# Performance work log

Measured on AMD Instinct MI355X. Metric: run time of the kernel, lower is better.

The kernel has to match this reference:

```python
import jax, jax.numpy as jnp
import numpy as np

N_NODES = 50000


def _gcn_conv(x, W, b, src, dst, n):
    # PyG GCNConv: h = x @ W, symmetric-normalized aggregation, then + bias.
    h = x @ W  # [N, out]
    deg = jax.ops.segment_sum(jnp.ones_like(dst, dtype=h.dtype), dst, num_segments=n)
    dinv = jnp.where(deg > 0, jax.lax.rsqrt(jnp.maximum(deg, 1e-12)), 0.0)
    norm = dinv[src] * dinv[dst]  # [E]
    msg = h[src] * norm[:, None]  # gather + scale, [E, out]
    out = jax.ops.segment_sum(msg, dst, num_segments=n)
    return out + b


def setup_inputs() -> dict:
    key = jax.random.key(0)
    ks = jax.random.split(key, 8)
    d_in, d_h, d_out = 256, 256, 128
    E = 800000
    x = jax.random.normal(ks[0], (N_NODES, d_in), dtype=jnp.float32)
    edge_index = jax.random.randint(ks[1], (2, E), 0, N_NODES, dtype=jnp.int64)
    def glorot(k, shape):
        lim = np.sqrt(6.0 / (shape[0] + shape[1]))
        return jax.random.uniform(k, shape, jnp.float32, -lim, lim)
    return {
        "x": x,
        "edge_index": edge_index,
        "W1": glorot(ks[2], (d_in, d_h)), "b1": jnp.zeros((d_h,), jnp.float32),
        "W2": glorot(ks[3], (d_h, d_h)), "b2": jnp.zeros((d_h,), jnp.float32),
        "W3": glorot(ks[4], (d_h, d_out)), "b3": jnp.zeros((d_out,), jnp.float32),
    }


def reference(x, edge_index, W1, b1, W2, b2, W3, b3):
    n = x.shape[0]
    # add self-loops once (PyG GCNConv default add_self_loops=True)
    loop = jnp.arange(n, dtype=edge_index.dtype)
    src = jnp.concatenate([edge_index[0], loop])
    dst = jnp.concatenate([edge_index[1], loop])
    h = _gcn_conv(x, W1, b1, src, dst, n)
    h = jax.nn.relu(h)  # dropout is identity in eval mode
    h = _gcn_conv(h, W2, b2, src, dst, n)
    h = jax.nn.relu(h)
    h = _gcn_conv(h, W3, b3, src, dst, n)
    return h
```

## Files before the change

### kernel.cpp

```cpp
#include <hip/hip_runtime.h>
#include <stdint.h>

typedef short v8s __attribute__((ext_vector_type(8)));
typedef float v4f __attribute__((ext_vector_type(4)));

__device__ inline float bf2f(unsigned short h) {
    union { unsigned u; float f; } c; c.u = ((unsigned)h) << 16; return c.f;
}
__device__ inline unsigned short f2bf(float f) {
    union { float f; unsigned u; } c; c.f = f;
    unsigned u = c.u;
    unsigned r = (u + 0x7FFFu + ((u >> 16) & 1u)) >> 16;
    return (unsigned short)r;
}
__device__ inline void gl_lds16(const unsigned short* g, unsigned short* l) {
    __builtin_amdgcn_global_load_lds(
        (const __attribute__((address_space(1))) unsigned int*)(g),
        (__attribute__((address_space(3))) unsigned int*)(l), 16, 0, 0);
}

__global__ void k_count(const int* __restrict__ dst, int E, int* __restrict__ cnt) {
    int e = blockIdx.x * 256 + threadIdx.x;
    if (e < E) atomicAdd(&cnt[dst[e]], 1);
}

__global__ void k_scan1(const int* __restrict__ cnt, int n, int* __restrict__ incl,
                        int* __restrict__ bsum) {
    __shared__ int sm[256];
    int t = threadIdx.x;
    int i = blockIdx.x * 256 + t;
    int v = (i < n) ? cnt[i] : 0;
    sm[t] = v; __syncthreads();
    for (int off = 1; off < 256; off <<= 1) {
        int add = (t >= off) ? sm[t - off] : 0;
        __syncthreads();
        sm[t] += add;
        __syncthreads();
    }
    if (i < n) incl[i] = sm[t];
    if (t == 255) bsum[blockIdx.x] = sm[255];
}

__global__ void k_scan2(const int* __restrict__ bsum, int nb, int* __restrict__ boff) {
    __shared__ int sm[256];
    int t = threadIdx.x;
    int v = (t < nb) ? bsum[t] : 0;
    sm[t] = v; __syncthreads();
    for (int off = 1; off < 256; off <<= 1) {
        int add = (t >= off) ? sm[t - off] : 0;
        __syncthreads();
        sm[t] += add;
        __syncthreads();
    }
    if (t < nb) boff[t] = sm[t] - v;
}

__global__ void k_scan3(const int* __restrict__ cnt, int n, const int* __restrict__ boff,
                        int* __restrict__ rs, float* __restrict__ dinv) {
    int i = blockIdx.x * 256 + threadIdx.x;
    if (i < n) {
        int c = cnt[i];
        rs[i] = rs[i] + boff[blockIdx.x] - c;
        dinv[i] = rsqrtf((float)(c + 1));
    }
}

__global__ void k_scatter(const int* __restrict__ src, const int* __restrict__ dst, int E,
                          const int* __restrict__ rs, int* __restrict__ cursor,
                          int* __restrict__ col) {
    int e = blockIdx.x * 256 + threadIdx.x;
    if (e < E) {
        int d = dst[e];
        int p = rs[d] + atomicAdd(&cursor[d], 1);
        col[p] = src[e];
    }
}

__global__ void k_cvt_x(const float* __restrict__ x, unsigned short* __restrict__ A,
                        int n, int mpad) {
    int g = blockIdx.x * 256 + threadIdx.x;
    int total = mpad * 64;
    if (g >= total) return;
    int row = g >> 6;
    float4 v;
    if (row < n) v = ((const float4*)x)[(size_t)g];
    else v = make_float4(0.f, 0.f, 0.f, 0.f);
    ushort4 o;
    o.x = f2bf(v.x); o.y = f2bf(v.y); o.z = f2bf(v.z); o.w = f2bf(v.w);
    ((ushort4*)A)[(size_t)g] = o;
}

__global__ void k_cvt_w3(const float* __restrict__ W1, const float* __restrict__ W2,
                         const float* __restrict__ W3, unsigned short* __restrict__ Wt) {
    int idx = blockIdx.x * 256 + threadIdx.x;
    const float* W; int base, N;
    if (idx < 65536)       { W = W1; base = 0;      N = 256; }
    else if (idx < 131072) { W = W2; base = 65536;  N = 256; }
    else                   { W = W3; base = 131072; N = 128; }
    int loc = idx - base;
    int nn = loc >> 8;
    int k = loc & 255;
    Wt[idx] = f2bf(W[(size_t)k * N + nn]);
}

__launch_bounds__(256, 2)
__global__ void k_gemm(const unsigned short* __restrict__ A,
                       const unsigned short* __restrict__ Wt,
                       unsigned short* __restrict__ Hs,
                       const float* __restrict__ dinv, int n, int N) {
    __shared__ unsigned short sA[128 * 32];
    __shared__ unsigned short sB[128 * 32];
    const int t = threadIdx.x;
    const int lane = t & 63;
    const int wave = t >> 6;
    const int wm = wave >> 1, wn = wave & 1;
    const int m0 = blockIdx.x * 128;
    const int n0 = blockIdx.y * 128;

    v4f acc[4][4];
#pragma unroll
    for (int i = 0; i < 4; i++)
#pragma unroll
        for (int j = 0; j < 4; j++)
#pragma unroll
            for (int r = 0; r < 4; r++) acc[i][j][r] = 0.f;

    const int c0 = t, c1 = t + 256;
    const int r0 = c0 >> 2, kc0 = (c0 & 3) * 8;
    const int r1 = c1 >> 2, kc1 = (c1 & 3) * 8;
    const size_t aBase0 = (size_t)(m0 + r0) * 256 + kc0;
    const size_t aBase1 = (size_t)(m0 + r1) * 256 + kc1;
    const size_t bBase0 = (size_t)(n0 + r0) * 256 + kc0;
    const size_t bBase1 = (size_t)(n0 + r1) * 256 + kc1;

    const int q = lane >> 4;
    const int lm = lane & 15;

    for (int k0 = 0; k0 < 256; k0 += 32) {
        __syncthreads();
        gl_lds16(A + aBase0 + k0, &sA[c0 * 8]);
        gl_lds16(A + aBase1 + k0, &sA[c1 * 8]);
        gl_lds16(Wt + bBase0 + k0, &sB[c0 * 8]);
        gl_lds16(Wt + bBase1 + k0, &sB[c1 * 8]);
        __syncthreads();

        v8s afr[4], bfr[4];
#pragma unroll
        for (int i = 0; i < 4; i++) {
            int r = wm * 64 + i * 16 + lm;
            afr[i] = *(const v8s*)&sA[r * 32 + q * 8];
        }
#pragma unroll
        for (int j = 0; j < 4; j++) {
            int nn = wn * 64 + j * 16 + lm;
            bfr[j] = *(const v8s*)&sB[nn * 32 + q * 8];
        }
#pragma unroll
        for (int i = 0; i < 4; i++)
#pragma unroll
            for (int j = 0; j < 4; j++)
                acc[i][j] = __builtin_amdgcn_mfma_f32_16x16x32_bf16(afr[i], bfr[j],
                                                                    acc[i][j], 0, 0, 0);
    }

#pragma unroll
    for (int i = 0; i < 4; i++) {
        int mbase = m0 + wm * 64 + i * 16 + q * 4;
#pragma unroll
        for (int r = 0; r < 4; r++) {
            int m = mbase + r;
            float s = (m < n) ? dinv[m] : 0.f;
#pragma unroll
            for (int j = 0; j < 4; j++) {
                int colI = n0 + wn * 64 + j * 16 + lm;
                Hs[(size_t)m * N + colI] = f2bf(acc[i][j][r] * s);
            }
        }
    }
}

template <int D, bool RELU, bool F32OUT>
__launch_bounds__(256, 8)
__global__ void k_agg(const unsigned short* __restrict__ Hs,
                      const int* __restrict__ rs, const int* __restrict__ cnt,
                      const int* __restrict__ col, const float* __restrict__ dinv,
                      const float* __restrict__ bias,
                      unsigned short* __restrict__ outb, float* __restrict__ outf,
                      int n, int nzero) {
    constexpr int LPN = D / 8;
    constexpr int NPG = 64 / LPN;
    const int lane = threadIdx.x & 63;
    const int i = blockIdx.x * 4 + (threadIdx.x >> 6);
    if (i >= n) return;
    const int g = lane / LPN;
    const int cl = lane % LPN;

    float acc[8];
#pragma unroll
    for (int k = 0; k < 8; k++) acc[k] = 0.f;

    auto acc8 = [&](uint4 q) {
        acc[0] += bf2f((unsigned short)(q.x & 0xffffu));
        acc[1] += bf2f((unsigned short)(q.x >> 16));
        acc[2] += bf2f((unsigned short)(q.y & 0xffffu));
        acc[3] += bf2f((unsigned short)(q.y >> 16));
        acc[4] += bf2f((unsigned short)(q.z & 0xffffu));
        acc[5] += bf2f((unsigned short)(q.z >> 16));
        acc[6] += bf2f((unsigned short)(q.w & 0xffffu));
        acc[7] += bf2f((unsigned short)(q.w >> 16));
    };

    const int s = rs[i], deg = cnt[i];
    const int T = deg + 1;
    const int Tpad = (T + NPG - 1) & ~(NPG - 1);

    for (int b = 0; b < Tpad; b += 64) {
        int t = b + lane;
        int v;
        if (t == 0) v = i;
        else if (t <= deg) v = col[s + t - 1];
        else v = nzero;
        int lim = min(64, Tpad - b);
        int t2 = 0;
        for (; t2 + 2 * NPG <= lim; t2 += 2 * NPG) {
            int c0 = __shfl(v, t2 + g);
            int c1 = __shfl(v, t2 + NPG + g);
            uint4 q0 = *(const uint4*)(Hs + (size_t)c0 * D + cl * 8);
            uint4 q1 = *(const uint4*)(Hs + (size_t)c1 * D + cl * 8);
            acc8(q0);
            acc8(q1);
        }
        if (t2 < lim) {
            int c0 = __shfl(v, t2 + g);
            uint4 q0 = *(const uint4*)(Hs + (size_t)c0 * D + cl * 8);
            acc8(q0);
        }
    }

#pragma unroll
    for (int off = LPN; off < 64; off <<= 1) {
#pragma unroll
        for (int k = 0; k < 8; k++) acc[k] += __shfl_xor(acc[k], off);
    }

    if (g == 0) {
        float di = dinv[i];
        float o[8];
#pragma unroll
        for (int k = 0; k < 8; k++) {
            o[k] = di * acc[k] + bias[cl * 8 + k];
            if (RELU) o[k] = fmaxf(o[k], 0.f);
        }
        if constexpr (F32OUT) {
            float4 a = make_float4(o[0], o[1], o[2], o[3]);
            float4 b = make_float4(o[4], o[5], o[6], o[7]);
            float* p = outf + (size_t)i * D + cl * 8;
            *(float4*)p = a;
            *(float4*)(p + 4) = b;
        } else {
            uint4 q;
            q.x = ((unsigned)f2bf(o[1]) << 16) | f2bf(o[0]);
            q.y = ((unsigned)f2bf(o[3]) << 16) | f2bf(o[2]);
            q.z = ((unsigned)f2bf(o[5]) << 16) | f2bf(o[4]);
            q.w = ((unsigned)f2bf(o[7]) << 16) | f2bf(o[6]);
            *(uint4*)(outb + (size_t)i * D + cl * 8) = q;
        }
    }
}

extern "C" void kernel_launch(void* const* d_in, const int* in_sizes, int n_in,
                              void* d_out, int out_size, void* d_ws, size_t ws_size,
                              hipStream_t stream) {
    const float* x  = (const float*)d_in[0];
    const int*   ei = (const int*)d_in[1];
    const float* W1 = (const float*)d_in[2];
    const float* b1 = (const float*)d_in[3];
    const float* W2 = (const float*)d_in[4];
    const float* b2 = (const float*)d_in[5];
    const float* W3 = (const float*)d_in[6];
    const float* b3 = (const float*)d_in[7];

    const int n = in_sizes[0] / 256;
    const int E = in_sizes[1] / 2;
    const int mpad = ((n + 127) / 128) * 128;

    char* ws = (char*)d_ws;
    size_t off = 0;
    auto alloc = [&](size_t bytes) -> void* {
        void* p = ws + off;
        off += (bytes + 255) & ~(size_t)255;
        return p;
    };
    int* cz       = (int*)alloc((size_t)2 * n * 4);
    int* cnt      = cz;
    int* cursor   = cz + n;
    int* rs       = (int*)alloc((size_t)n * 4);
    float* dinv   = (float*)alloc((size_t)n * 4);
    int* bsum     = (int*)alloc(256 * 4);
    int* boff     = (int*)alloc(256 * 4);
    int* col      = (int*)alloc((size_t)E * 4);
    unsigned short* Wt = (unsigned short*)alloc((size_t)163840 * 2);
    unsigned short* W1t = Wt;
    unsigned short* W2t = Wt + 65536;
    unsigned short* W3t = Wt + 131072;
    unsigned short* bufA = (unsigned short*)alloc((size_t)mpad * 256 * 2);
    unsigned short* bufB = (unsigned short*)alloc((size_t)mpad * 256 * 2);
    (void)ws_size; (void)n_in; (void)out_size;

    const int* srcp = ei;
    const int* dstp = ei + E;
    const int gE = (E + 255) / 256;
    const int gN = (n + 255) / 256;

    hipMemsetAsync(cz, 0, (size_t)2 * n * 4, stream);

    k_count<<<gE, 256, 0, stream>>>(dstp, E, cnt);
    k_scan1<<<gN, 256, 0, stream>>>(cnt, n, rs, bsum);
    k_scan2<<<1, 256, 0, stream>>>(bsum, gN, boff);
    k_scan3<<<gN, 256, 0, stream>>>(cnt, n, boff, rs, dinv);
    k_scatter<<<gE, 256, 0, stream>>>(srcp, dstp, E, rs, cursor, col);

    k_cvt_x<<<(mpad * 64 + 255) / 256, 256, 0, stream>>>(x, bufA, n, mpad);
    k_cvt_w3<<<640, 256, 0, stream>>>(W1, W2, W3, Wt);

    const int gAgg = (n + 3) / 4;
    dim3 gg1(mpad / 128, 2);
    k_gemm<<<gg1, 256, 0, stream>>>(bufA, W1t, bufB, dinv, n, 256);
    k_agg<256, true, false><<<gAgg, 256, 0, stream>>>(bufB, rs, cnt, col, dinv, b1,
                                                      bufA, nullptr, n, n);
    k_gemm<<<gg1, 256, 0, stream>>>(bufA, W2t, bufB, dinv, n, 256);
    k_agg<256, true, false><<<gAgg, 256, 0, stream>>>(bufB, rs, cnt, col, dinv, b2,
                                                      bufA, nullptr, n, n);
    dim3 gg3(mpad / 128, 1);
    k_gemm<<<gg3, 256, 0, stream>>>(bufA, W3t, bufB, dinv, n, 128);
    k_agg<128, false, true><<<gAgg, 256, 0, stream>>>(bufB, rs, cnt, col, dinv, b3,
                                                      nullptr, (float*)d_out, n, n);
}
```

Baseline: 397.3 us.

## Fuse preprocessing kernels, record edge slots in count pass, widen aggregation unroll

Merges the degree count, x conversion and weight transpose into one launch. The count pass now saves each edge's atomic return value as its slot, so the scatter pass no longer needs a second atomic and the cursor buffer is dropped. The aggregation kernel unrolls its gather loop by four and accumulates in float2 vectors, and the GEMM launch bound is raised from 2 to 4 blocks per SM. This trades an extra E-sized seq buffer and more register pressure for fewer launches, fewer atomics and more loads in flight.

```diff
diff --git a/kernel.cpp b/kernel.cpp
--- a/kernel.cpp
+++ b/kernel.cpp
@@ -3,6 +3,7 @@
 
 typedef short v8s __attribute__((ext_vector_type(8)));
 typedef float v4f __attribute__((ext_vector_type(4)));
+typedef float v2f __attribute__((ext_vector_type(2)));
 
 __device__ inline float bf2f(unsigned short h) {
     union { unsigned u; float f; } c; c.u = ((unsigned)h) << 16; return c.f;
@@ -19,9 +20,39 @@
         (__attribute__((address_space(3))) unsigned int*)(l), 16, 0, 0);
 }
 
-__global__ void k_count(const int* __restrict__ dst, int E, int* __restrict__ cnt) {
-    int e = blockIdx.x * 256 + threadIdx.x;
-    if (e < E) atomicAdd(&cnt[dst[e]], 1);
+__global__ void k_pre1(const int* __restrict__ dst, int E,
+                       int* __restrict__ cnt, int* __restrict__ seq,
+                       const float* __restrict__ x, unsigned short* __restrict__ A,
+                       int n, int mpad,
+                       const float* __restrict__ W1, const float* __restrict__ W2,
+                       const float* __restrict__ W3, unsigned short* __restrict__ Wt,
+                       int gE, int gX) {
+    int b = blockIdx.x;
+    if (b < gE) {
+        int e = b * 256 + threadIdx.x;
+        if (e < E) seq[e] = atomicAdd(&cnt[dst[e]], 1);
+    } else if (b < gE + gX) {
+        int g = (b - gE) * 256 + threadIdx.x;
+        int total = mpad * 64;
+        if (g >= total) return;
+        int row = g >> 6;
+        float4 v;
+        if (row < n) v = ((const float4*)x)[(size_t)g];
+        else v = make_float4(0.f, 0.f, 0.f, 0.f);
+        ushort4 o;
+        o.x = f2bf(v.x); o.y = f2bf(v.y); o.z = f2bf(v.z); o.w = f2bf(v.w);
+        ((ushort4*)A)[(size_t)g] = o;
+    } else {
+        int idx = (b - gE - gX) * 256 + threadIdx.x;
+        const float* W; int base, N;
+        if (idx < 65536)       { W = W1; base = 0;      N = 256; }
+        else if (idx < 131072) { W = W2; base = 65536;  N = 256; }
+        else                   { W = W3; base = 131072; N = 128; }
+        int loc = idx - base;
+        int nn = loc >> 8;
+        int k = loc & 255;
+        Wt[idx] = f2bf(W[(size_t)k * N + nn]);
+    }
 }
 
 __global__ void k_scan1(const int* __restrict__ cnt, int n, int* __restrict__ incl,
@@ -65,45 +96,14 @@
     }
 }
 
-__global__ void k_scatter(const int* __restrict__ src, const int* __restrict__ dst, int E,
-                          const int* __restrict__ rs, int* __restrict__ cursor,
-                          int* __restrict__ col) {
+__global__ void k_scatter2(const int* __restrict__ src, const int* __restrict__ dst,
+                           const int* __restrict__ seq, int E,
+                           const int* __restrict__ rs, int* __restrict__ col) {
     int e = blockIdx.x * 256 + threadIdx.x;
-    if (e < E) {
-        int d = dst[e];
-        int p = rs[d] + atomicAdd(&cursor[d], 1);
-        col[p] = src[e];
-    }
-}
-
-__global__ void k_cvt_x(const float* __restrict__ x, unsigned short* __restrict__ A,
-                        int n, int mpad) {
-    int g = blockIdx.x * 256 + threadIdx.x;
-    int total = mpad * 64;
-    if (g >= total) return;
-    int row = g >> 6;
-    float4 v;
-    if (row < n) v = ((const float4*)x)[(size_t)g];
-    else v = make_float4(0.f, 0.f, 0.f, 0.f);
-    ushort4 o;
-    o.x = f2bf(v.x); o.y = f2bf(v.y); o.z = f2bf(v.z); o.w = f2bf(v.w);
-    ((ushort4*)A)[(size_t)g] = o;
-}
-
-__global__ void k_cvt_w3(const float* __restrict__ W1, const float* __restrict__ W2,
-                         const float* __restrict__ W3, unsigned short* __restrict__ Wt) {
-    int idx = blockIdx.x * 256 + threadIdx.x;
-    const float* W; int base, N;
-    if (idx < 65536)       { W = W1; base = 0;      N = 256; }
-    else if (idx < 131072) { W = W2; base = 65536;  N = 256; }
-    else                   { W = W3; base = 131072; N = 128; }
-    int loc = idx - base;
-    int nn = loc >> 8;
-    int k = loc & 255;
-    Wt[idx] = f2bf(W[(size_t)k * N + nn]);
-}
-
-__launch_bounds__(256, 2)
+    if (e < E) col[rs[dst[e]] + seq[e]] = src[e];
+}
+
+__launch_bounds__(256, 4)
 __global__ void k_gemm(const unsigned short* __restrict__ A,
                        const unsigned short* __restrict__ Wt,
                        unsigned short* __restrict__ Hs,
@@ -195,21 +195,20 @@
     const int g = lane / LPN;
     const int cl = lane % LPN;
 
-    float acc[8];
-#pragma unroll
-    for (int k = 0; k < 8; k++) acc[k] = 0.f;
-
-    auto acc8 = [&](uint4 q) {
-        acc[0] += bf2f((unsigned short)(q.x & 0xffffu));
-        acc[1] += bf2f((unsigned short)(q.x >> 16));
-        acc[2] += bf2f((unsigned short)(q.y & 0xffffu));
-        acc[3] += bf2f((unsigned short)(q.y >> 16));
-        acc[4] += bf2f((unsigned short)(q.z & 0xffffu));
-        acc[5] += bf2f((unsigned short)(q.z >> 16));
-        acc[6] += bf2f((unsigned short)(q.w & 0xffffu));
-        acc[7] += bf2f((unsigned short)(q.w >> 16));
+    v2f acc[4];
+#pragma unroll
+    for (int k = 0; k < 4; k++) acc[k] = (v2f){0.f, 0.f};
+
+    auto accq = [&](unsigned u, int k) {
+        union { unsigned uu; float f; } lo, hi;
+        lo.uu = u << 16;
+        hi.uu = u & 0xffff0000u;
+        v2f t; t[0] = lo.f; t[1] = hi.f;
+        acc[k] += t;
     };
-
+    auto acc16 = [&](uint4 q) { accq(q.x, 0); accq(q.y, 1); accq(q.z, 2); accq(q.w, 3); };
+
+    const unsigned short* base = Hs + cl * 8;
     const int s = rs[i], deg = cnt[i];
     const int T = deg + 1;
     const int Tpad = (T + NPG - 1) & ~(NPG - 1);
@@ -222,41 +221,49 @@
         else v = nzero;
         int lim = min(64, Tpad - b);
         int t2 = 0;
-        for (; t2 + 2 * NPG <= lim; t2 += 2 * NPG) {
+        for (; t2 + 4 * NPG <= lim; t2 += 4 * NPG) {
+            int c0 = __shfl(v, t2 + 0 * NPG + g);
+            int c1 = __shfl(v, t2 + 1 * NPG + g);
+            int c2 = __shfl(v, t2 + 2 * NPG + g);
+            int c3 = __shfl(v, t2 + 3 * NPG + g);
+            uint4 q0 = *(const uint4*)(base + (size_t)c0 * D);
+            uint4 q1 = *(const uint4*)(base + (size_t)c1 * D);
+            uint4 q2 = *(const uint4*)(base + (size_t)c2 * D);
+            uint4 q3 = *(const uint4*)(base + (size_t)c3 * D);
+            acc16(q0); acc16(q1); acc16(q2); acc16(q3);
+        }
+        for (; t2 + NPG <= lim; t2 += NPG) {
             int c0 = __shfl(v, t2 + g);
-            int c1 = __shfl(v, t2 + NPG + g);
-            uint4 q0 = *(const uint4*)(Hs + (size_t)c0 * D + cl * 8);
-            uint4 q1 = *(const uint4*)(Hs + (size_t)c1 * D + cl * 8);
-            acc8(q0);
-            acc8(q1);
-        }
-        if (t2 < lim) {
-            int c0 = __shfl(v, t2 + g);
-            uint4 q0 = *(const uint4*)(Hs + (size_t)c0 * D + cl * 8);
-            acc8(q0);
+            uint4 q0 = *(const uint4*)(base + (size_t)c0 * D);
+            acc16(q0);
         }
     }
 
 #pragma unroll
     for (int off = LPN; off < 64; off <<= 1) {
 #pragma unroll
-        for (int k = 0; k < 8; k++) acc[k] += __shfl_xor(acc[k], off);
+        for (int k = 0; k < 4; k++) {
+            acc[k][0] += __shfl_xor(acc[k][0], off);
+            acc[k][1] += __shfl_xor(acc[k][1], off);
+        }
     }
 
     if (g == 0) {
         float di = dinv[i];
         float o[8];
 #pragma unroll
-        for (int k = 0; k < 8; k++) {
-            o[k] = di * acc[k] + bias[cl * 8 + k];
-            if (RELU) o[k] = fmaxf(o[k], 0.f);
+        for (int k = 0; k < 4; k++) {
+            o[2 * k + 0] = di * acc[k][0] + bias[cl * 8 + 2 * k + 0];
+            o[2 * k + 1] = di * acc[k][1] + bias[cl * 8 + 2 * k + 1];
+        }
+        if (RELU) {
+#pragma unroll
+            for (int k = 0; k < 8; k++) o[k] = fmaxf(o[k], 0.f);
         }
         if constexpr (F32OUT) {
-            float4 a = make_float4(o[0], o[1], o[2], o[3]);
-            float4 b = make_float4(o[4], o[5], o[6], o[7]);
             float* p = outf + (size_t)i * D + cl * 8;
-            *(float4*)p = a;
-            *(float4*)(p + 4) = b;
+            *(float4*)p = make_float4(o[0], o[1], o[2], o[3]);
+            *(float4*)(p + 4) = make_float4(o[4], o[5], o[6], o[7]);
         } else {
             uint4 q;
             q.x = ((unsigned)f2bf(o[1]) << 16) | f2bf(o[0]);
@@ -291,13 +298,12 @@
         off += (bytes + 255) & ~(size_t)255;
         return p;
     };
-    int* cz       = (int*)alloc((size_t)2 * n * 4);
-    int* cnt      = cz;
-    int* cursor   = cz + n;
+    int* cnt      = (int*)alloc((size_t)n * 4);
     int* rs       = (int*)alloc((size_t)n * 4);
     float* dinv   = (float*)alloc((size_t)n * 4);
     int* bsum     = (int*)alloc(256 * 4);
     int* boff     = (int*)alloc(256 * 4);
+    int* seq      = (int*)alloc((size_t)E * 4);
     int* col      = (int*)alloc((size_t)E * 4);
     unsigned short* Wt = (unsigned short*)alloc((size_t)163840 * 2);
     unsigned short* W1t = Wt;
@@ -311,17 +317,17 @@
     const int* dstp = ei + E;
     const int gE = (E + 255) / 256;
     const int gN = (n + 255) / 256;
-
-    hipMemsetAsync(cz, 0, (size_t)2 * n * 4, stream);
-
-    k_count<<<gE, 256, 0, stream>>>(dstp, E, cnt);
+    const int gX = (mpad * 64 + 255) / 256;
+    const int gW = 640;
+
+    hipMemsetAsync(cnt, 0, (size_t)n * 4, stream);
+
+    k_pre1<<<gE + gX + gW, 256, 0, stream>>>(dstp, E, cnt, seq, x, bufA, n, mpad,
+                                             W1, W2, W3, Wt, gE, gX);
     k_scan1<<<gN, 256, 0, stream>>>(cnt, n, rs, bsum);
     k_scan2<<<1, 256, 0, stream>>>(bsum, gN, boff);
     k_scan3<<<gN, 256, 0, stream>>>(cnt, n, boff, rs, dinv);
-    k_scatter<<<gE, 256, 0, stream>>>(srcp, dstp, E, rs, cursor, col);
-
-    k_cvt_x<<<(mpad * 64 + 255) / 256, 256, 0, stream>>>(x, bufA, n, mpad);
-    k_cvt_w3<<<640, 256, 0, stream>>>(W1, W2, W3, Wt);
+    k_scatter2<<<gE, 256, 0, stream>>>(srcp, dstp, seq, E, rs, col);
 
     const int gAgg = (n + 3) / 4;
     dim3 gg1(mpad / 128, 2);
```

New measurement: 354.9 us. 1.12x faster.
